# Kernel optimization log

Measured on AMD Instinct MI355X. Metric: run time of the kernel, lower is better.

Reference implementation:

```python
import jax, jax.numpy as jnp
import numpy as np

B, N, H, HEADS, NBINS = 64, 256, 512, 8, 3
DK = H // HEADS
NEG = -1e12

def setup_inputs() -> dict:
    key = jax.random.key(0)
    ks = jax.random.split(key, 20)
    def lin(k, out_d, in_d):
        w = jax.random.normal(k, (out_d, in_d), jnp.float32) * (1.0 / np.sqrt(in_d))
        b = jnp.zeros((out_d,), jnp.float32)
        return w, b
    x = jax.random.normal(ks[0], (B, N, H), jnp.float32)
    dist = jax.random.uniform(ks[1], (B, N - 1, N - 1), jnp.float32, 0.0, 10.0)
    dist_bar = jnp.sort(jax.random.uniform(ks[2], (B, NBINS), jnp.float32, 1.0, 9.0), axis=-1)
    mask = jnp.ones((B, N, N), jnp.float32)
    Wq, bq = lin(ks[3], H, H)
    Wk, bk = lin(ks[4], H, H)
    Wv, bv = lin(ks[5], H, H)
    Wa = jnp.stack([lin(ks[6 + i], H, H)[0] for i in range(NBINS)])  # [NBINS,H,H]
    ba = jnp.zeros((NBINS, H), jnp.float32)
    Ws1, bs1 = lin(ks[10], H, NBINS * H)
    Ws2, bs2 = lin(ks[11], H, H)
    gamma = jnp.ones((H,), jnp.float32)
    beta = jnp.zeros((H,), jnp.float32)
    return dict(x=x, dist=dist, dist_bar=dist_bar, mask=mask, Wq=Wq, bq=bq, Wk=Wk, bk=bk,
                Wv=Wv, bv=bv, Wa=Wa, ba=ba, Ws1=Ws1, bs1=bs1, Ws2=Ws2, bs2=bs2,
                gamma=gamma, beta=beta)

def reference(x, dist, dist_bar, mask, Wq, bq, Wk, bk, Wv, bv, Wa, ba, Ws1, bs1, Ws2, bs2, gamma, beta):
    residual = x
    def proj(x, W, b):  # torch Linear: x @ W.T + b
        return jnp.einsum('bnd,od->bno', x, W) + b
    def heads(t):  # [B,N,H] -> [B,heads,N,dk]
        return t.reshape(B, N, HEADS, DK).transpose(0, 2, 1, 3)
    q, k, v = heads(proj(x, Wq, bq)), heads(proj(x, Wk, bk)), heads(proj(x, Wv, bv))
    scores = jnp.einsum('bhnd,bhmd->bhnm', q, k) / jnp.sqrt(jnp.float32(DK))  # [B,heads,N,N]
    # padding mask (shape [B,1,N,N] != scores shape -> masked_fill(mask==0))
    scores = jnp.where(mask[:, None] == 0, NEG, scores)
    # new_dist: super node row/col = 1, interior = dist
    new_dist = jnp.ones((B, 1, N, N), jnp.float32).at[:, :, 1:, 1:].set(dist[:, None])
    multi_out, attn_list = [], []
    for i in range(NBINS):
        cut = dist_bar[:, i][:, None, None, None]          # per-batch threshold
        dm = new_dist < cut                                 # [B,1,N,N]
        dm = dm.at[:, :, 0, :].set(True).at[:, :, :, 0].set(True)
        sd = jnp.where(dm, scores, NEG)
        attn = jax.nn.softmax(sd, axis=-1)                  # dropout: eval mode
        attn_list.append(attn)
        multi_out.append(jnp.einsum('bhnm,bhmd->bhnd', attn, v))
    x_cat = jnp.concatenate([
        jnp.einsum('bnd,od->bno', multi_out[i].transpose(0, 2, 1, 3).reshape(B, N, H), Wa[i]) + ba[i]
        for i in range(NBINS)], axis=-1)                    # [B,N,NBINS*H]
    h = jax.nn.silu(jnp.einsum('bnd,od->bno', x_cat, Ws1) + bs1)
    h = jnp.einsum('bnd,od->bno', h, Ws2) + bs2
    h = h + residual
    mu = jnp.mean(h, axis=-1, keepdims=True)
    var = jnp.var(h, axis=-1, keepdims=True)
    out = (h - mu) / jnp.sqrt(var + 1e-6) * gamma + beta
    return (out, jnp.stack(attn_list))
```

## Files before the change

### kernel.cpp

```cpp
#include <hip/hip_runtime.h>
#include <cstddef>

#define NEGV (-1e12f)


typedef __attribute__((ext_vector_type(4))) float f32x4;
typedef __attribute__((ext_vector_type(8))) __bf16 bf16x8;

__device__ __forceinline__ unsigned short f2bf(float f) {
  union { float f; unsigned u; } v; v.f = f;
  unsigned r = v.u + 0x7FFFu + ((v.u >> 16) & 1u);
  return (unsigned short)(r >> 16);
}

#define GLDS16(gp, lp)                                                      \
  __builtin_amdgcn_global_load_lds(                                         \
      (const __attribute__((address_space(1))) void*)(gp),                  \
      (__attribute__((address_space(3))) void*)(lp), 16, 0, 0)

__global__ __launch_bounds__(256) void msa_prep(
    const float* __restrict__ x, const float* __restrict__ Wq,
    const float* __restrict__ Wk, const float* __restrict__ Wv,
    const float* __restrict__ Ws2, const float* __restrict__ Ws1,
    const float* __restrict__ Wa, const float* __restrict__ bq,
    const float* __restrict__ bk, const float* __restrict__ bv,
    const float* __restrict__ ba, const float* __restrict__ bs1,
    const float* __restrict__ dist, const float* __restrict__ dist_bar,
    const float* __restrict__ maskg,
    unsigned short* __restrict__ xb, unsigned short* __restrict__ Wqkvb,
    unsigned short* __restrict__ Ws2b, unsigned short* __restrict__ Wcatb,
    float* __restrict__ bcomb, float* __restrict__ bqkv,
    unsigned long long* __restrict__ bits) {
  __shared__ float As[16][68];
  __shared__ float Bs[16][68];
  const int blk = blockIdx.x;
  const int tid = threadIdx.x;
  if (blk < 8192) {
    int i = blk * 256 + tid;
    float4 v = ((const float4*)x)[i];
    ushort4 o; o.x = f2bf(v.x); o.y = f2bf(v.y); o.z = f2bf(v.z); o.w = f2bf(v.w);
    ((ushort4*)xb)[i] = o;
    return;
  }
  if (blk < 8960) {
    int sel = (blk - 8192) >> 8;
    int i = ((blk - 8192) & 255) * 256 + tid;
    const float* src = (sel == 0) ? Wq : (sel == 1) ? Wk : Wv;
    unsigned short* dst = Wqkvb + (size_t)sel * 262144;
    float4 v = ((const float4*)src)[i];
    ushort4 o; o.x = f2bf(v.x); o.y = f2bf(v.y); o.z = f2bf(v.z); o.w = f2bf(v.w);
    ((ushort4*)dst)[i] = o;
    return;
  }
  if (blk < 9216) {
    int i = (blk - 8960) * 256 + tid;
    float4 v = ((const float4*)Ws2)[i];
    ushort4 o; o.x = f2bf(v.x); o.y = f2bf(v.y); o.z = f2bf(v.z); o.w = f2bf(v.w);
    ((ushort4*)Ws2b)[i] = o;
    return;
  }
  if (blk < 9408) {
    const int t = blk - 9216;
    const int i = t >> 6;
    const int ob = ((t >> 3) & 7) * 64, cb = (t & 7) * 64;
    const int tx = tid & 15, ty = tid >> 4;
    float acc[4][4] = {};
    for (int kt = 0; kt < 512; kt += 16) {
      __syncthreads();
      {
        int o = tid & 63, e4 = (tid >> 6) * 4;
        float4 a4 = *(const float4*)&Ws1[(size_t)(ob + o) * 1536 + i * 512 + kt + e4];
        As[e4 + 0][o] = a4.x; As[e4 + 1][o] = a4.y;
        As[e4 + 2][o] = a4.z; As[e4 + 3][o] = a4.w;
      }
      {
        int e = tid & 15, c4 = (tid >> 4) * 4;
        float4 b4 = *(const float4*)&Wa[((size_t)i << 18) + (size_t)(kt + e) * 512 + cb + c4];
        *(float4*)&Bs[e][c4] = b4;
      }
      __syncthreads();
#pragma unroll
      for (int k = 0; k < 16; ++k) {
        float a[4], bb[4];
        *(float4*)a = *(const float4*)&As[k][ty * 4];
        *(float4*)bb = *(const float4*)&Bs[k][tx * 4];
#pragma unroll
        for (int r = 0; r < 4; ++r)
#pragma unroll
          for (int c = 0; c < 4; ++c) acc[r][c] += a[r] * bb[c];
      }
    }
#pragma unroll
    for (int r = 0; r < 4; ++r)
#pragma unroll
      for (int c = 0; c < 4; ++c)
        Wcatb[(size_t)(ob + ty * 4 + r) * 1536 + i * 512 + cb + tx * 4 + c] =
            f2bf(acc[r][c]);
    return;
  }
  if (blk < 9410) {
    int o = (blk - 9408) * 256 + tid;
    float acc = bs1[o];
    for (int cidx = 0; cidx < 1536; ++cidx)
      acc += Ws1[(size_t)o * 1536 + cidx] * ba[cidx];
    bcomb[o] = acc;
    return;
  }
  if (blk < 9411) {
    for (int i = tid; i < 1536; i += 256)
      bqkv[i] = (i < 512) ? bq[i] : (i < 1024) ? bk[i - 512] : bv[i - 1024];
    return;
  }
  {
    const int gw = (blk - 9411) * 4 + (tid >> 6);
    const int lane = tid & 63;
    const int b = gw >> 8, row = gw & 255;
    const float cut0 = dist_bar[b * 3 + 0];
    const float cut1 = dist_bar[b * 3 + 1];
    const float cut2 = dist_bar[b * 3 + 2];
    const float* mrow = maskg + (size_t)b * 65536 + (size_t)row * 256;
    const int rj = (row == 0) ? 1 : row;
    const float* drow = dist + (size_t)b * 65025 + (size_t)(rj - 1) * 255;
    unsigned long long* out = bits + (size_t)gw * 12;
#pragma unroll
    for (int cc = 0; cc < 4; ++cc) {
      const int col = cc * 64 + lane;
      const int cj = (col == 0) ? 1 : col;
      float dv = drow[cj - 1];
      bool sup = (row == 0) || (col == 0);
      bool mk = (mrow[col] != 0.f);
      if (sup) dv = -1e30f;
      unsigned long long b0 = __ballot(mk && (dv < cut0));
      unsigned long long b1 = __ballot(mk && (dv < cut1));
      unsigned long long b2 = __ballot(mk && (dv < cut2));
      if (lane == 0) { out[cc] = b0; out[4 + cc] = b1; out[8 + cc] = b2; }
    }
  }
}

template <int ACT, int RES, int OBF, int BK>
__global__ __launch_bounds__(256) void msa_gemm_mfma(
    const unsigned short* __restrict__ A, int lda,
    const unsigned short* __restrict__ W, int ldw,
    const float* __restrict__ bias, const float* __restrict__ resid,
    void* __restrict__ Cout, int ldc, int Kdim) {
  constexpr int KSUB = BK / 32;
  constexpr int RPC = BK / 8;
  constexpr int CPT = (128 * RPC) / 256;
  __shared__ __align__(16) unsigned short Asm_[2][128 * BK];
  __shared__ __align__(16) unsigned short Bsm_[2][128 * BK];
  const int tid = threadIdx.x;
  const int lane = tid & 63, wv = tid >> 6;
  const int m0 = blockIdx.x * 128, n0 = blockIdx.y * 128;
  const int wr = wv >> 1, wc = wv & 1;
  const int fr = lane & 15, fq = lane >> 4;
  f32x4 acc[4][4] = {};
  const unsigned short* Ag[CPT];
  const unsigned short* Wg[CPT];
#pragma unroll
  for (int i = 0; i < CPT; ++i) {
    int c = tid + i * 256;
    int row = c / RPC, j = c % RPC;
    Ag[i] = A + (size_t)(m0 + row) * lda + j * 8;
    Wg[i] = W + (size_t)(n0 + row) * ldw + j * 8;
  }
#pragma unroll
  for (int i = 0; i < CPT; ++i) {
    GLDS16(Ag[i], &Asm_[0][(tid + i * 256) * 8]);
    GLDS16(Wg[i], &Bsm_[0][(tid + i * 256) * 8]);
  }
  __syncthreads();
  int cur = 0;
  for (int kt = 0; kt < Kdim; kt += BK) {
    if (kt + BK < Kdim) {
      const int nx = cur ^ 1, k2 = kt + BK;
#pragma unroll
      for (int i = 0; i < CPT; ++i) {
        GLDS16(Ag[i] + k2, &Asm_[nx][(tid + i * 256) * 8]);
        GLDS16(Wg[i] + k2, &Bsm_[nx][(tid + i * 256) * 8]);
      }
    }
#pragma unroll
    for (int ks = 0; ks < KSUB; ++ks) {
      bf16x8 af[4], bfr[4];
#pragma unroll
      for (int mf = 0; mf < 4; ++mf)
        af[mf] = *(const bf16x8*)&Asm_[cur][(wr * 64 + mf * 16 + fr) * BK + ks * 32 + fq * 8];
#pragma unroll
      for (int nf = 0; nf < 4; ++nf)
        bfr[nf] = *(const bf16x8*)&Bsm_[cur][(wc * 64 + nf * 16 + fr) * BK + ks * 32 + fq * 8];
#pragma unroll
      for (int mf = 0; mf < 4; ++mf)
#pragma unroll
        for (int nf = 0; nf < 4; ++nf)
          acc[mf][nf] = __builtin_amdgcn_mfma_f32_16x16x32_bf16(
              af[mf], bfr[nf], acc[mf][nf], 0, 0, 0);
    }
    __syncthreads();
    cur ^= 1;
  }
#pragma unroll
  for (int mf = 0; mf < 4; ++mf) {
#pragma unroll
    for (int nf = 0; nf < 4; ++nf) {
      const int n = n0 + wc * 64 + nf * 16 + fr;
      const float bval = bias[n];
#pragma unroll
      for (int r = 0; r < 4; ++r) {
        const int m = m0 + wr * 64 + mf * 16 + fq * 4 + r;
        float val = acc[mf][nf][r] + bval;
        if (ACT == 1) val = val / (1.f + __expf(-val));
        if (RES == 1) val += resid[(size_t)m * ldc + n];
        if (OBF == 1)
          ((unsigned short*)Cout)[(size_t)m * ldc + n] = f2bf(val);
        else
          ((float*)Cout)[(size_t)m * ldc + n] = val;
      }
    }
  }
}

__global__ __launch_bounds__(512) void msa_fused(
    const unsigned short* __restrict__ qkvb,
    const unsigned long long* __restrict__ bits,
    float* __restrict__ attn_out, unsigned short* __restrict__ mob) {
  const int blk = blockIdx.x;
  const int b = (blk & 7) * 8 + (blk >> 6);
  const int h = (blk >> 3) & 7;
  __shared__ __align__(16) unsigned short Kl[256][72];
  __shared__ __align__(16) unsigned short Vt[64][264];
  __shared__ __align__(16) unsigned short Pl[8][16][256];
  const int tid = threadIdx.x;
  const int wv = tid >> 6, lane = tid & 63;
  const int l15 = lane & 15, fq = lane >> 4;
  {
    const unsigned short* kgp = qkvb + (size_t)(b * 256) * 1536 + 512 + h * 64;
#pragma unroll
    for (int i = 0; i < 4; ++i) {
      int s = tid + i * 512;
      int row = s >> 3, c8 = (s & 7) << 3;
      *(uint4*)&Kl[row][c8] = *(const uint4*)&kgp[(size_t)row * 1536 + c8];
    }
  }
  {
    int rv = tid & 255, half = tid >> 8;
    const unsigned short* vgp =
        qkvb + (size_t)(b * 256 + rv) * 1536 + 1024 + h * 64 + half * 32;
#pragma unroll
    for (int j4 = 0; j4 < 4; ++j4) {
      unsigned short tmp[8];
      *(uint4*)tmp = *(const uint4*)&vgp[j4 * 8];
#pragma unroll
      for (int j = 0; j < 8; ++j) Vt[half * 32 + j4 * 8 + j][rv] = tmp[j];
    }
  }
  __syncthreads();
  char* plbase = (char*)&Pl[wv][0][0];
  const int swz = ((l15 & 1) << 6) | ((l15 & 2) << 4);
#pragma unroll
  for (int mf = 0; mf < 2; ++mf) {
    const int r0 = wv * 32 + mf * 16;
    const int q = r0 + l15;
    const unsigned short* qgp =
        qkvb + (size_t)(b * 256 + q) * 1536 + h * 64 + fq * 8;
    bf16x8 aq0 = *(const bf16x8*)qgp;
    bf16x8 aq1 = *(const bf16x8*)(qgp + 32);
    f32x4 accs[16];
#pragma unroll
    for (int nt = 0; nt < 16; ++nt) {
      bf16x8 bk0 = *(const bf16x8*)&Kl[nt * 16 + l15][fq * 8];
      bf16x8 bk1 = *(const bf16x8*)&Kl[nt * 16 + l15][32 + fq * 8];
      f32x4 a = {};
      a = __builtin_amdgcn_mfma_f32_16x16x32_bf16(bk0, aq0, a, 0, 0, 0);
      a = __builtin_amdgcn_mfma_f32_16x16x32_bf16(bk1, aq1, a, 0, 0, 0);
      accs[nt] = a;
    }
    const unsigned long long* brow = bits + (size_t)(b * 256 + q) * 12;
#pragma unroll
    for (int bin = 0; bin < 3; ++bin) {
      const unsigned long long w0 = brow[bin * 4 + 0];
      const unsigned long long w1 = brow[bin * 4 + 1];
      const unsigned long long w2 = brow[bin * 4 + 2];
      const unsigned long long w3 = brow[bin * 4 + 3];
      f32x4 p[16];
      float m = -3e38f;
#pragma unroll
      for (int nt = 0; nt < 16; ++nt) {
        unsigned long long w = (nt < 4) ? w0 : (nt < 8) ? w1 : (nt < 12) ? w2 : w3;
#pragma unroll
        for (int r = 0; r < 4; ++r) {
          unsigned keep = (unsigned)(w >> (16 * (nt & 3) + 4 * fq + r)) & 1u;
          float sv = accs[nt][r] * 0.125f;
          float v = keep ? sv : NEGV;
          p[nt][r] = v;
          m = fmaxf(m, v);
        }
      }
      m = fmaxf(m, __shfl_xor(m, 16));
      m = fmaxf(m, __shfl_xor(m, 32));
      float sum = 0.f;
#pragma unroll
      for (int nt = 0; nt < 16; ++nt)
#pragma unroll
        for (int r = 0; r < 4; ++r) {
          p[nt][r] = __expf(p[nt][r] - m);
          sum += p[nt][r];
        }
      sum += __shfl_xor(sum, 16);
      sum += __shfl_xor(sum, 32);
      const float inv = 1.f / sum;
      float* prow = attn_out + ((size_t)((bin * 64 + b) * 8 + h)) * 65536 +
                    (size_t)q * 256;
#pragma unroll
      for (int nt = 0; nt < 16; ++nt) {
        float v0 = p[nt][0] * inv, v1 = p[nt][1] * inv;
        float v2 = p[nt][2] * inv, v3 = p[nt][3] * inv;
        *(float4*)(prow + nt * 16 + fq * 4) = make_float4(v0, v1, v2, v3);
        unsigned short u[4];
        u[0] = f2bf(v0); u[1] = f2bf(v1); u[2] = f2bf(v2); u[3] = f2bf(v3);
        int wb = (l15 << 9) | (nt << 5) | (fq << 3);
        *(uint2*)(plbase + (wb ^ swz)) = *(const uint2*)u;
      }
      asm volatile("s_waitcnt lgkmcnt(0)" ::: "memory");
      __builtin_amdgcn_sched_barrier(0);
      f32x4 acco[4] = {};
#pragma unroll
      for (int c = 0; c < 8; ++c) {
        int rb = (l15 << 9) | (c << 6) | (fq << 4);
        bf16x8 pa = *(const bf16x8*)(plbase + (rb ^ swz));
#pragma unroll
        for (int nf = 0; nf < 4; ++nf) {
          bf16x8 bv = *(const bf16x8*)&Vt[nf * 16 + l15][c * 32 + fq * 8];
          acco[nf] = __builtin_amdgcn_mfma_f32_16x16x32_bf16(pa, bv, acco[nf], 0, 0, 0);
        }
      }
#pragma unroll
      for (int nf = 0; nf < 4; ++nf)
#pragma unroll
        for (int r = 0; r < 4; ++r)
          mob[((size_t)(b * 256 + r0 + fq * 4 + r) * 3 + bin) * 512 +
              h * 64 + nf * 16 + l15] = f2bf(acco[nf][r]);
      asm volatile("s_waitcnt lgkmcnt(0)" ::: "memory");
      __builtin_amdgcn_sched_barrier(0);
    }
  }
}

__global__ __launch_bounds__(256) void msa_mlp2ln(
    const unsigned short* __restrict__ h1b, const unsigned short* __restrict__ Ws2b,
    const float* __restrict__ bs2, const float* __restrict__ x,
    const float* __restrict__ gamma, const float* __restrict__ beta,
    float* __restrict__ outp) {
  __shared__ __align__(16) unsigned short Al[32 * 32];
  __shared__ __align__(16) unsigned short Bl[512 * 32];
  __shared__ float red[2][2][32];
  const int tid = threadIdx.x;
  const int lane = tid & 63, wv = tid >> 6;
  const int wr = wv >> 1, wc = wv & 1;
  const int l15 = lane & 15, fq = lane >> 4;
  const int m0 = blockIdx.x * 32;
  f32x4 acc[16] = {};
  for (int kt = 0; kt < 512; kt += 32) {
    if (tid < 128) {
      int row = tid >> 2, c8 = (tid & 3) * 8;
      GLDS16(h1b + (size_t)(m0 + row) * 512 + kt + c8, &Al[tid * 8]);
    }
#pragma unroll
    for (int i = 0; i < 8; ++i) {
      int c = tid + i * 256;
      int row = c >> 2, c8 = (c & 3) * 8;
      GLDS16(Ws2b + (size_t)row * 512 + kt + c8, &Bl[c * 8]);
    }
    __syncthreads();
    bf16x8 af = *(const bf16x8*)&Al[(wr * 16 + l15) * 32 + fq * 8];
#pragma unroll
    for (int nt = 0; nt < 16; ++nt) {
      bf16x8 bfr = *(const bf16x8*)&Bl[(wc * 256 + nt * 16 + l15) * 32 + fq * 8];
      acc[nt] = __builtin_amdgcn_mfma_f32_16x16x32_bf16(af, bfr, acc[nt], 0, 0, 0);
    }
    __syncthreads();
  }
  float vals[16][4];
#pragma unroll
  for (int nt = 0; nt < 16; ++nt) {
    const int n = wc * 256 + nt * 16 + l15;
    const float bval = bs2[n];
#pragma unroll
    for (int r = 0; r < 4; ++r) {
      const int m = m0 + wr * 16 + fq * 4 + r;
      vals[nt][r] = acc[nt][r] + bval + x[(size_t)m * 512 + n];
    }
  }
  const int ridx = wr * 16 + fq * 4;
#pragma unroll
  for (int r = 0; r < 4; ++r) {
    float s = 0.f;
#pragma unroll
    for (int nt = 0; nt < 16; ++nt) s += vals[nt][r];
    s += __shfl_xor(s, 1); s += __shfl_xor(s, 2);
    s += __shfl_xor(s, 4); s += __shfl_xor(s, 8);
    if (l15 == 0) red[0][wc][ridx + r] = s;
  }
  __syncthreads();
  float mu[4];
#pragma unroll
  for (int r = 0; r < 4; ++r)
    mu[r] = (red[0][0][ridx + r] + red[0][1][ridx + r]) * (1.f / 512.f);
#pragma unroll
  for (int r = 0; r < 4; ++r) {
    float s = 0.f;
#pragma unroll
    for (int nt = 0; nt < 16; ++nt) {
      float d = vals[nt][r] - mu[r];
      s += d * d;
    }
    s += __shfl_xor(s, 1); s += __shfl_xor(s, 2);
    s += __shfl_xor(s, 4); s += __shfl_xor(s, 8);
    if (l15 == 0) red[1][wc][ridx + r] = s;
  }
  __syncthreads();
  float iv[4];
#pragma unroll
  for (int r = 0; r < 4; ++r) {
    float var = (red[1][0][ridx + r] + red[1][1][ridx + r]) * (1.f / 512.f);
    iv[r] = 1.f / sqrtf(var + 1e-6f);
  }
#pragma unroll
  for (int nt = 0; nt < 16; ++nt) {
    const int n = wc * 256 + nt * 16 + l15;
    const float g = gamma[n], be = beta[n];
#pragma unroll
    for (int r = 0; r < 4; ++r) {
      const int m = m0 + wr * 16 + fq * 4 + r;
      outp[(size_t)m * 512 + n] = (vals[nt][r] - mu[r]) * iv[r] * g + be;
    }
  }
}

extern "C" void kernel_launch(void* const* d_in, const int* in_sizes, int n_in,
                              void* d_out, int out_size, void* d_ws, size_t ws_size,
                              hipStream_t stream) {
  (void)in_sizes; (void)n_in; (void)out_size; (void)ws_size;
  const float* x        = (const float*)d_in[0];
  const float* dist     = (const float*)d_in[1];
  const float* dist_bar = (const float*)d_in[2];
  const float* mask     = (const float*)d_in[3];
  const float* Wq  = (const float*)d_in[4];  const float* bq  = (const float*)d_in[5];
  const float* Wk  = (const float*)d_in[6];  const float* bk  = (const float*)d_in[7];
  const float* Wv  = (const float*)d_in[8];  const float* bv  = (const float*)d_in[9];
  const float* Wa  = (const float*)d_in[10]; const float* ba  = (const float*)d_in[11];
  const float* Ws1 = (const float*)d_in[12]; const float* bs1 = (const float*)d_in[13];
  const float* Ws2 = (const float*)d_in[14]; const float* bs2 = (const float*)d_in[15];
  const float* gamma = (const float*)d_in[16]; const float* beta = (const float*)d_in[17];

  char* w8 = (char*)d_ws;
  const size_t SZ = 8388608;
  unsigned short* qkvb = (unsigned short*)(w8 + 0);
  unsigned short* mob  = (unsigned short*)(w8 + 50331648);
  unsigned short* xb   = (unsigned short*)(w8 + 100663296);
  unsigned short* Wqkvb= (unsigned short*)(w8 + 117440512);
  unsigned short* Ws2b = (unsigned short*)(w8 + 119013376);
  unsigned short* Wcatb= (unsigned short*)(w8 + 119537664);
  float* bcomb = (float*)(w8 + 121110528);
  float* bqkv  = (float*)(w8 + 121112576);
  unsigned long long* bits = (unsigned long long*)(w8 + 121118720);
  unsigned short* h1b = qkvb;
  float* outp = (float*)d_out;
  float* attn = outp + SZ;

  msa_prep<<<13507, 256, 0, stream>>>(x, Wq, Wk, Wv, Ws2, Ws1, Wa, bq, bk, bv,
                                      ba, bs1, dist, dist_bar, mask,
                                      xb, Wqkvb, Ws2b, Wcatb, bcomb, bqkv, bits);

  msa_gemm_mfma<0, 0, 1, 32><<<dim3(128, 12), 256, 0, stream>>>(
      xb, 512, Wqkvb, 512, bqkv, nullptr, qkvb, 1536, 512);

  msa_fused<<<512, 512, 0, stream>>>(qkvb, bits, attn, mob);

  msa_gemm_mfma<1, 0, 1, 64><<<dim3(128, 4), 256, 0, stream>>>(
      mob, 1536, Wcatb, 1536, bcomb, nullptr, h1b, 512, 1536);

  msa_mlp2ln<<<512, 256, 0, stream>>>(h1b, Ws2b, bs2, x, gamma, beta, outp);
}
```

Measured before the change: 325.3 us.

## Split weight-fold tiles, warp-reduce bias fold, prescale Q, nontemporal attn stores

The Wa·Ws1 weight-fold section of the prep kernel now uses 32-row tiles, doubling its block count for more parallelism. The bias fold moves from one thread per output to one wavefront per output with a shuffle reduction, giving coalesced reads. The 1/sqrt(dk) scale is applied to Q in the QKV GEMM epilogue instead of per score in softmax, and the fp32 attention probabilities are written with nontemporal stores to avoid polluting the cache. Prescaling Q before the bf16 cast is exact, since it is a power-of-two scale.

```diff
diff --git a/kernel.cpp b/kernel.cpp
--- a/kernel.cpp
+++ b/kernel.cpp
@@ -31,7 +31,7 @@
     unsigned short* __restrict__ Ws2b, unsigned short* __restrict__ Wcatb,
     float* __restrict__ bcomb, float* __restrict__ bqkv,
     unsigned long long* __restrict__ bits) {
-  __shared__ float As[16][68];
+  __shared__ float As[16][36];
   __shared__ float Bs[16][68];
   const int blk = blockIdx.x;
   const int tid = threadIdx.x;
@@ -59,16 +59,17 @@
     ((ushort4*)Ws2b)[i] = o;
     return;
   }
-  if (blk < 9408) {
+  if (blk < 9600) {
     const int t = blk - 9216;
-    const int i = t >> 6;
-    const int ob = ((t >> 3) & 7) * 64, cb = (t & 7) * 64;
+    const int i = t >> 7;
+    const int rem = t & 127;
+    const int ob = (rem >> 3) * 32, cb = (rem & 7) * 64;
     const int tx = tid & 15, ty = tid >> 4;
-    float acc[4][4] = {};
+    float acc[2][4] = {};
     for (int kt = 0; kt < 512; kt += 16) {
       __syncthreads();
-      {
-        int o = tid & 63, e4 = (tid >> 6) * 4;
+      if (tid < 128) {
+        int o = tid >> 2, e4 = (tid & 3) * 4;
         float4 a4 = *(const float4*)&Ws1[(size_t)(ob + o) * 1536 + i * 512 + kt + e4];
         As[e4 + 0][o] = a4.x; As[e4 + 1][o] = a4.y;
         As[e4 + 2][o] = a4.z; As[e4 + 3][o] = a4.w;
@@ -81,38 +82,48 @@
       __syncthreads();
 #pragma unroll
       for (int k = 0; k < 16; ++k) {
-        float a[4], bb[4];
-        *(float4*)a = *(const float4*)&As[k][ty * 4];
+        float a0 = As[k][ty * 2], a1 = As[k][ty * 2 + 1];
+        float bb[4];
         *(float4*)bb = *(const float4*)&Bs[k][tx * 4];
 #pragma unroll
-        for (int r = 0; r < 4; ++r)
-#pragma unroll
-          for (int c = 0; c < 4; ++c) acc[r][c] += a[r] * bb[c];
-      }
-    }
-#pragma unroll
-    for (int r = 0; r < 4; ++r)
+        for (int c = 0; c < 4; ++c) {
+          acc[0][c] += a0 * bb[c];
+          acc[1][c] += a1 * bb[c];
+        }
+      }
+    }
+#pragma unroll
+    for (int rr = 0; rr < 2; ++rr)
 #pragma unroll
       for (int c = 0; c < 4; ++c)
-        Wcatb[(size_t)(ob + ty * 4 + r) * 1536 + i * 512 + cb + tx * 4 + c] =
-            f2bf(acc[r][c]);
-    return;
-  }
-  if (blk < 9410) {
-    int o = (blk - 9408) * 256 + tid;
-    float acc = bs1[o];
-    for (int cidx = 0; cidx < 1536; ++cidx)
-      acc += Ws1[(size_t)o * 1536 + cidx] * ba[cidx];
-    bcomb[o] = acc;
-    return;
-  }
-  if (blk < 9411) {
+        Wcatb[(size_t)(ob + ty * 2 + rr) * 1536 + i * 512 + cb + tx * 4 + c] =
+            f2bf(acc[rr][c]);
+    return;
+  }
+  if (blk < 9728) {
+    const int o = (blk - 9600) * 4 + (tid >> 6);
+    const int lane = tid & 63;
+    const float* row = Ws1 + (size_t)o * 1536;
+    float s = 0.f;
+#pragma unroll
+    for (int c0 = 0; c0 < 1536; c0 += 256) {
+      s += row[c0 + lane] * ba[c0 + lane];
+      s += row[c0 + 64 + lane] * ba[c0 + 64 + lane];
+      s += row[c0 + 128 + lane] * ba[c0 + 128 + lane];
+      s += row[c0 + 192 + lane] * ba[c0 + 192 + lane];
+    }
+#pragma unroll
+    for (int off = 32; off > 0; off >>= 1) s += __shfl_xor(s, off);
+    if (lane == 0) bcomb[o] = bs1[o] + s;
+    return;
+  }
+  if (blk < 9729) {
     for (int i = tid; i < 1536; i += 256)
       bqkv[i] = (i < 512) ? bq[i] : (i < 1024) ? bk[i - 512] : bv[i - 1024];
     return;
   }
   {
-    const int gw = (blk - 9411) * 4 + (tid >> 6);
+    const int gw = (blk - 9729) * 4 + (tid >> 6);
     const int lane = tid & 63;
     const int b = gw >> 8, row = gw & 255;
     const float cut0 = dist_bar[b * 3 + 0];
@@ -138,7 +149,7 @@
   }
 }
 
-template <int ACT, int RES, int OBF, int BK>
+template <int ACT, int RES, int OBF, int BK, int SQ>
 __global__ __launch_bounds__(256) void msa_gemm_mfma(
     const unsigned short* __restrict__ A, int lda,
     const unsigned short* __restrict__ W, int ldw,
@@ -209,6 +220,7 @@
       for (int r = 0; r < 4; ++r) {
         const int m = m0 + wr * 64 + mf * 16 + fq * 4 + r;
         float val = acc[mf][nf][r] + bval;
+        if (SQ == 1 && n < 512) val *= 0.125f;
         if (ACT == 1) val = val / (1.f + __expf(-val));
         if (RES == 1) val += resid[(size_t)m * ldc + n];
         if (OBF == 1)
@@ -290,7 +302,7 @@
 #pragma unroll
         for (int r = 0; r < 4; ++r) {
           unsigned keep = (unsigned)(w >> (16 * (nt & 3) + 4 * fq + r)) & 1u;
-          float sv = accs[nt][r] * 0.125f;
+          float sv = accs[nt][r];
           float v = keep ? sv : NEGV;
           p[nt][r] = v;
           m = fmaxf(m, v);
@@ -315,7 +327,8 @@
       for (int nt = 0; nt < 16; ++nt) {
         float v0 = p[nt][0] * inv, v1 = p[nt][1] * inv;
         float v2 = p[nt][2] * inv, v3 = p[nt][3] * inv;
-        *(float4*)(prow + nt * 16 + fq * 4) = make_float4(v0, v1, v2, v3);
+        f32x4 st = {v0, v1, v2, v3};
+        __builtin_nontemporal_store(st, (f32x4*)(prow + nt * 16 + fq * 4));
         unsigned short u[4];
         u[0] = f2bf(v0); u[1] = f2bf(v1); u[2] = f2bf(v2); u[3] = f2bf(v3);
         int wb = (l15 << 9) | (nt << 5) | (fq << 3);
@@ -468,16 +481,16 @@
   float* outp = (float*)d_out;
   float* attn = outp + SZ;
 
-  msa_prep<<<13507, 256, 0, stream>>>(x, Wq, Wk, Wv, Ws2, Ws1, Wa, bq, bk, bv,
+  msa_prep<<<13825, 256, 0, stream>>>(x, Wq, Wk, Wv, Ws2, Ws1, Wa, bq, bk, bv,
                                       ba, bs1, dist, dist_bar, mask,
                                       xb, Wqkvb, Ws2b, Wcatb, bcomb, bqkv, bits);
 
-  msa_gemm_mfma<0, 0, 1, 32><<<dim3(128, 12), 256, 0, stream>>>(
+  msa_gemm_mfma<0, 0, 1, 32, 1><<<dim3(128, 12), 256, 0, stream>>>(
       xb, 512, Wqkvb, 512, bqkv, nullptr, qkvb, 1536, 512);
 
   msa_fused<<<512, 512, 0, stream>>>(qkvb, bits, attn, mob);
 
-  msa_gemm_mfma<1, 0, 1, 64><<<dim3(128, 4), 256, 0, stream>>>(
+  msa_gemm_mfma<1, 0, 1, 64, 0><<<dim3(128, 4), 256, 0, stream>>>(
       mob, 1536, Wcatb, 1536, bcomb, nullptr, h1b, 512, 1536);
 
   msa_mlp2ln<<<512, 256, 0, stream>>>(h1b, Ws2b, bs2, x, gamma, beta, outp);
```

Measured after the change: 307.1 us. -5.6%, faster.
